# Kernel optimization log

Hardware: AMD Instinct MI355X
Metric: run time of the kernel (lower is better)

The kernel has to match this reference:

```python
import jax, jax.numpy as jnp
import numpy as np

CUTOFF = 5.0           # module init kwarg
NSYS, NAT = 64, 1000   # 64 systems of 1000 atoms each
BOX = 21.544           # cubic box edge -> ~0.1 atoms/A^3 (water-like density)
MAX_PAIRS = 2_200_000


def setup_inputs() -> dict:
    key = jax.random.key(0)
    coords = jax.random.uniform(key, (NSYS * NAT, 3), dtype=jnp.float32) * BOX
    isys = jnp.repeat(jnp.arange(NSYS, dtype=jnp.int32), NAT)
    natoms = jnp.full((NSYS,), NAT, dtype=jnp.int32)
    return {"coordinates": coords, "isys": isys, "natoms": natoms}


def reference(coordinates, isys, natoms):
    # Fixed-capacity cutoff neighbor list (no PBC branch), faithful to
    # GraphGeneratorFixed: half-list (i<j, same system), squared distances d12,
    # compacted into a MAX_PAIRS buffer padded with padding_value=N, then
    # symmetrized by concatenation.
    nsys = natoms.shape[0]
    n = coordinates.shape[0]
    nat = n // nsys                      # equal-sized systems (static)
    padding_value = n
    cutoff2 = jnp.float32(CUTOFF * CUTOFF)

    x = coordinates.reshape(nsys, nat, 3)                 # [S, nat, 3]
    sq = jnp.sum(x * x, axis=-1)                          # [S, nat]
    gram = jnp.einsum('sid,sjd->sij', x, x)               # [S, nat, nat]
    d12 = sq[:, :, None] + sq[:, None, :] - 2.0 * gram    # squared distances

    triu = jnp.triu(jnp.ones((nat, nat), dtype=bool), k=1)  # i < j half-list
    mask = (d12 < cutoff2) & triu[None, :, :]             # [S, nat, nat]
    mflat = mask.reshape(-1)                              # [S*nat*nat]
    npairs = jnp.sum(mflat)

    # stream-compaction: position of each kept pair in the output buffer
    pos = jnp.cumsum(mflat.astype(jnp.int32)) - 1
    sel = jnp.where(mflat, pos, MAX_PAIRS)                # OOB -> dropped
    flat_idx = jnp.arange(nsys * nat * nat, dtype=jnp.int32)
    idx_buf = jnp.full((MAX_PAIRS,), -1, dtype=jnp.int32).at[sel].set(
        flat_idx, mode='drop')

    valid = idx_buf >= 0
    ib = jnp.maximum(idx_buf, 0)
    s = ib // (nat * nat)
    rem = ib % (nat * nat)
    i = rem // nat
    j = rem % nat
    src = jnp.where(valid, s * nat + i, padding_value)
    dst = jnp.where(valid, s * nat + j, padding_value)
    d12_sel = jnp.where(valid, d12.reshape(-1)[ib], cutoff2)

    # symmetrize (directed graph), as in the original
    edge_src = jnp.concatenate([src, dst])
    edge_dst = jnp.concatenate([dst, src])
    d12_out = jnp.concatenate([d12_sel, d12_sel])
    return edge_src, edge_dst, d12_out, npairs
```

## Files before the change

kernel.cpp:

```cpp
#include <hip/hip_runtime.h>

#define NSYS 64
#define NAT  1000
#define NTOT (NSYS * NAT)
#define MP   2200000
#define CUT2 25.0f
#define PADV 64000.0f
#define SCAN_BLOCKS 250
#define CAP  104
#define EB   512
#define LCN  1152
#define NROWS 512
#define POSB  4096

__device__ __forceinline__ float dist2f(float xi, float yi, float zi,
                                        float xj, float yj, float zj) {
    float dx = xi - xj, dy = yi - yj, dz = zi - zj;
    return fmaf(dz, dz, fmaf(dy, dy, dx * dx));
}

__device__ __forceinline__ int mbcnt(unsigned long long m) {
    unsigned lo = __builtin_amdgcn_mbcnt_lo((unsigned)m, 0u);
    return (int)__builtin_amdgcn_mbcnt_hi((unsigned)(m >> 32), lo);
}

__device__ __forceinline__ int emit_group(uint2* __restrict__ q, int running,
                                          bool k, int j, int r, float d,
                                          unsigned long long m) {
    if (k) {
        int rank = running + mbcnt(m);
        if (rank < CAP)
            q[rank] = make_uint2((unsigned)(j - r), __float_as_uint(d));
    }
    return running + (int)__popcll(m);
}

__global__ __launch_bounds__(1024) void k_eval(const float* __restrict__ coords,
                                               int* __restrict__ counts,
                                               uint2* __restrict__ qbuf) {
    __shared__ float4 lc[LCN];
    int s      = blockIdx.x >> 3;
    int stripe = blockIdx.x & 7;
    const float* cs = coords + s * (NAT * 3);
    for (int a = threadIdx.x; a < LCN; a += 1024)
        lc[a] = (a < NAT)
              ? make_float4(cs[3 * a], cs[3 * a + 1], cs[3 * a + 2], 0.0f)
              : make_float4(1.0e30f, 1.0e30f, 1.0e30f, 0.0f);
    __syncthreads();
    int w    = threadIdx.x >> 6;
    int lane = threadIdx.x & 63;
    int W    = stripe * 16 + w;
#pragma unroll
    for (int t = 0; t < 2; t++) {
        int Q = t ? (255 - W) : W;
        if (Q > 249) continue;
        int r0 = Q * 4;
        float4 a0 = lc[r0];
        float4 a1 = lc[r0 + 1];
        float4 a2 = lc[r0 + 2];
        float4 a3 = lc[r0 + 3];
        int gb = __builtin_amdgcn_readfirstlane(s * NAT + r0);
        uint2* q0 = qbuf + (size_t)gb * CAP;
        uint2* q1 = q0 + CAP;
        uint2* q2 = q1 + CAP;
        uint2* q3 = q2 + CAP;
        int run0 = 0, run1 = 0, run2 = 0, run3 = 0;
        {
            int j = r0 + 1 + lane;
            float4 c = lc[j];
            float d0 = dist2f(a0.x, a0.y, a0.z, c.x, c.y, c.z);
            float d1 = dist2f(a1.x, a1.y, a1.z, c.x, c.y, c.z);
            float d2 = dist2f(a2.x, a2.y, a2.z, c.x, c.y, c.z);
            float d3 = dist2f(a3.x, a3.y, a3.z, c.x, c.y, c.z);
            bool in = j < NAT;
            bool k0 = in && (d0 < CUT2);
            bool k1 = in && (j > r0 + 1) && (d1 < CUT2);
            bool k2 = in && (j > r0 + 2) && (d2 < CUT2);
            bool k3 = in && (j > r0 + 3) && (d3 < CUT2);
            unsigned long long m0 = __ballot(k0);
            unsigned long long m1 = __ballot(k1);
            unsigned long long m2 = __ballot(k2);
            unsigned long long m3 = __ballot(k3);
            run0 = emit_group(q0, run0, k0, j, r0,     d0, m0);
            run1 = emit_group(q1, run1, k1, j, r0 + 1, d1, m1);
            run2 = emit_group(q2, run2, k2, j, r0 + 2, d2, m2);
            run3 = emit_group(q3, run3, k3, j, r0 + 3, d3, m3);
        }
        int jb = r0 + 65;
        for (; jb + 127 < NAT; jb += 128) {
            int j = jb + lane;
            float4 c0 = lc[j];
            float4 c1 = lc[j + 64];
            float d00 = dist2f(a0.x, a0.y, a0.z, c0.x, c0.y, c0.z);
            float d10 = dist2f(a1.x, a1.y, a1.z, c0.x, c0.y, c0.z);
            float d20 = dist2f(a2.x, a2.y, a2.z, c0.x, c0.y, c0.z);
            float d30 = dist2f(a3.x, a3.y, a3.z, c0.x, c0.y, c0.z);
            bool k00 = d00 < CUT2;
            bool k10 = d10 < CUT2;
            bool k20 = d20 < CUT2;
            bool k30 = d30 < CUT2;
            unsigned long long m00 = __ballot(k00);
            unsigned long long m10 = __ballot(k10);
            unsigned long long m20 = __ballot(k20);
            unsigned long long m30 = __ballot(k30);
            run0 = emit_group(q0, run0, k00, j, r0,     d00, m00);
            run1 = emit_group(q1, run1, k10, j, r0 + 1, d10, m10);
            run2 = emit_group(q2, run2, k20, j, r0 + 2, d20, m20);
            run3 = emit_group(q3, run3, k30, j, r0 + 3, d30, m30);
            float d01 = dist2f(a0.x, a0.y, a0.z, c1.x, c1.y, c1.z);
            float d11 = dist2f(a1.x, a1.y, a1.z, c1.x, c1.y, c1.z);
            float d21 = dist2f(a2.x, a2.y, a2.z, c1.x, c1.y, c1.z);
            float d31 = dist2f(a3.x, a3.y, a3.z, c1.x, c1.y, c1.z);
            bool k01 = d01 < CUT2;
            bool k11 = d11 < CUT2;
            bool k21 = d21 < CUT2;
            bool k31 = d31 < CUT2;
            unsigned long long m01 = __ballot(k01);
            unsigned long long m11 = __ballot(k11);
            unsigned long long m21 = __ballot(k21);
            unsigned long long m31 = __ballot(k31);
            run0 = emit_group(q0, run0, k01, j + 64, r0,     d01, m01);
            run1 = emit_group(q1, run1, k11, j + 64, r0 + 1, d11, m11);
            run2 = emit_group(q2, run2, k21, j + 64, r0 + 2, d21, m21);
            run3 = emit_group(q3, run3, k31, j + 64, r0 + 3, d31, m31);
        }
        for (; jb < NAT; jb += 64) {
            int j = jb + lane;
            float4 c = lc[j];
            float d0 = dist2f(a0.x, a0.y, a0.z, c.x, c.y, c.z);
            float d1 = dist2f(a1.x, a1.y, a1.z, c.x, c.y, c.z);
            float d2 = dist2f(a2.x, a2.y, a2.z, c.x, c.y, c.z);
            float d3 = dist2f(a3.x, a3.y, a3.z, c.x, c.y, c.z);
            bool in = j < NAT;
            bool k0 = in && (d0 < CUT2);
            bool k1 = in && (d1 < CUT2);
            bool k2 = in && (d2 < CUT2);
            bool k3 = in && (d3 < CUT2);
            unsigned long long m0 = __ballot(k0);
            unsigned long long m1 = __ballot(k1);
            unsigned long long m2 = __ballot(k2);
            unsigned long long m3 = __ballot(k3);
            run0 = emit_group(q0, run0, k0, j, r0,     d0, m0);
            run1 = emit_group(q1, run1, k1, j, r0 + 1, d1, m1);
            run2 = emit_group(q2, run2, k2, j, r0 + 2, d2, m2);
            run3 = emit_group(q3, run3, k3, j, r0 + 3, d3, m3);
        }
        if (lane == 0)
            *(int4*)(counts + gb) = make_int4(run0, run1, run2, run3);
    }
}

__global__ __launch_bounds__(256) void k_scan_a(const int* __restrict__ counts,
                                                int* __restrict__ offs,
                                                int* __restrict__ bsum) {
    __shared__ int wsum[4];
    int t = threadIdx.x, lane = t & 63, wid = t >> 6;
    int g = blockIdx.x * 256 + t;
    int v = counts[g];
    int x = v;
#pragma unroll
    for (int off = 1; off < 64; off <<= 1) {
        int u = __shfl_up(x, off);
        if (lane >= off) x += u;
    }
    if (lane == 63) wsum[wid] = x;
    __syncthreads();
    int base = 0;
    if (wid > 0) base += wsum[0];
    if (wid > 1) base += wsum[1];
    if (wid > 2) base += wsum[2];
    offs[g] = base + x - v;
    if (t == 255) bsum[blockIdx.x] = base + x;
}

__global__ __launch_bounds__(1024) void k_emit(const int* __restrict__ offs,
                                               const int* __restrict__ bsum,
                                               const uint2* __restrict__ qbuf,
                                               float* __restrict__ out) {
    __shared__ int bpre[256];
    __shared__ int lgoff[NROWS + 1];
    __shared__ int sh_r0, sh_tot;
    int t = threadIdx.x;
    int v = 0;
    if (t < 256) {
        v = (t < SCAN_BLOCKS) ? bsum[t] : 0;
        bpre[t] = v;
    }
    __syncthreads();
    for (int off = 1; off < 256; off <<= 1) {
        int u = 0;
        if (t < 256 && t >= off) u = bpre[t - off];
        __syncthreads();
        if (t < 256) bpre[t] += u;
        __syncthreads();
    }
    int incl = (t < 256) ? bpre[t] : 0;
    __syncthreads();
    if (t < 256) bpre[t] = incl - v;
    if (t == 255) sh_tot = incl;
    __syncthreads();
    int total = sh_tot;

    int p0 = blockIdx.x * POSB;
    if (t == 0) {
        int lo = 0, hi = NTOT;
        while (lo < hi) {
            int mid = (lo + hi + 1) >> 1;
            int g = (mid < NTOT) ? offs[mid] + bpre[mid >> 8] : total;
            if (g <= p0) lo = mid; else hi = mid - 1;
        }
        sh_r0 = lo;
    }
    __syncthreads();
    int r0 = sh_r0;
    if (t <= NROWS) {
        int r = r0 + t;
        lgoff[t] = (r < NTOT) ? offs[r] + bpre[r >> 8] : total;
    }
    __syncthreads();

    if (blockIdx.x == 0 && t == 0) out[6 * MP] = (float)total;
    int valid = total < MP ? total : MP;

    int p4 = p0 + t * 4;
    if (p4 >= MP) return;
    int k = 0;
    for (int step = 256; step; step >>= 1) {
        int nk = k + step;
        if (nk <= NROWS - 1 && lgoff[nk] <= p4) k = nk;
    }
    float fs[4], fd[4], dd[4];
#pragma unroll
    for (int e = 0; e < 4; e++) {
        int p = p4 + e;
        if (p < valid) {
            while (k < NROWS - 1 && lgoff[k + 1] <= p) k++;
            int row = r0 + k;
            int local = p - lgoff[k];
            if (local > CAP - 1) local = CAP - 1;
            uint2 rec = qbuf[(size_t)row * CAP + local];
            fs[e] = (float)row;
            fd[e] = (float)(row + (int)rec.x);
            dd[e] = __uint_as_float(rec.y);
        } else {
            fs[e] = PADV; fd[e] = PADV; dd[e] = CUT2;
        }
    }
    if (p4 + 4 <= MP) {
        float4 vs = {fs[0], fs[1], fs[2], fs[3]};
        float4 vd = {fd[0], fd[1], fd[2], fd[3]};
        float4 vv = {dd[0], dd[1], dd[2], dd[3]};
        *(float4*)(out + p4)          = vs;
        *(float4*)(out + MP + p4)     = vd;
        *(float4*)(out + 2 * MP + p4) = vd;
        *(float4*)(out + 3 * MP + p4) = vs;
        *(float4*)(out + 4 * MP + p4) = vv;
        *(float4*)(out + 5 * MP + p4) = vv;
    } else {
#pragma unroll
        for (int e = 0; e < 4; e++) {
            int p = p4 + e;
            if (p < MP) {
                out[p]          = fs[e];
                out[MP + p]     = fd[e];
                out[2 * MP + p] = fd[e];
                out[3 * MP + p] = fs[e];
                out[4 * MP + p] = dd[e];
                out[5 * MP + p] = dd[e];
            }
        }
    }
}

extern "C" void kernel_launch(void* const* d_in, const int* in_sizes, int n_in,
                              void* d_out, int out_size, void* d_ws, size_t ws_size,
                              hipStream_t stream) {
    const float* coords = (const float*)d_in[0];
    float* out = (float*)d_out;

    int*   counts = (int*)d_ws;
    int*   offs   = counts + NTOT;
    int*   bsum   = offs + NTOT;
    uint2* qbuf   = (uint2*)(bsum + 256);

    int emit_blocks = (MP + POSB - 1) / POSB;
    k_eval<<<EB, 1024, 0, stream>>>(coords, counts, qbuf);
    k_scan_a<<<SCAN_BLOCKS, 256, 0, stream>>>(counts, offs, bsum);
    k_emit<<<emit_blocks, 1024, 0, stream>>>(offs, bsum, qbuf, out);
}
```

Measured before the change: 108.3 us.

## Store 16-bit neighbor offsets and recompute distances in emit kernel

The intermediate per-row queue now holds a 16-bit column offset instead of an 8-byte (offset, distance) record, which cuts queue write and read traffic by a factor of four. The emit kernel recomputes the squared distance from the coordinates, which adds gathered coordinate loads that should mostly hit cache. The shared coordinate tile is padded further so the tail loop and its bounds checks can be dropped, and out-of-range columns are filtered by the sentinel coordinates instead. Recomputing the distance with a different formula than the reference may cause small rounding differences.

Result: no change. 106.3 us (-1.9%).

```diff
diff --git a/kernel.cpp b/kernel.cpp
--- a/kernel.cpp
+++ b/kernel.cpp
@@ -9,7 +9,7 @@
 #define SCAN_BLOCKS 250
 #define CAP  104
 #define EB   512
-#define LCN  1152
+#define LCN  1216
 #define NROWS 512
 #define POSB  4096
 
@@ -24,20 +24,20 @@
     return (int)__builtin_amdgcn_mbcnt_hi((unsigned)(m >> 32), lo);
 }
 
-__device__ __forceinline__ int emit_group(uint2* __restrict__ q, int running,
-                                          bool k, int j, int r, float d,
+__device__ __forceinline__ int emit_group(unsigned short* __restrict__ q,
+                                          int running, bool k, int dj,
                                           unsigned long long m) {
     if (k) {
         int rank = running + mbcnt(m);
         if (rank < CAP)
-            q[rank] = make_uint2((unsigned)(j - r), __float_as_uint(d));
+            q[rank] = (unsigned short)dj;
     }
     return running + (int)__popcll(m);
 }
 
 __global__ __launch_bounds__(1024) void k_eval(const float* __restrict__ coords,
                                                int* __restrict__ counts,
-                                               uint2* __restrict__ qbuf) {
+                                               unsigned short* __restrict__ qbuf) {
     __shared__ float4 lc[LCN];
     int s      = blockIdx.x >> 3;
     int stripe = blockIdx.x & 7;
@@ -60,10 +60,10 @@
         float4 a2 = lc[r0 + 2];
         float4 a3 = lc[r0 + 3];
         int gb = __builtin_amdgcn_readfirstlane(s * NAT + r0);
-        uint2* q0 = qbuf + (size_t)gb * CAP;
-        uint2* q1 = q0 + CAP;
-        uint2* q2 = q1 + CAP;
-        uint2* q3 = q2 + CAP;
+        unsigned short* q0 = qbuf + (size_t)gb * CAP;
+        unsigned short* q1 = q0 + CAP;
+        unsigned short* q2 = q1 + CAP;
+        unsigned short* q3 = q2 + CAP;
         int run0 = 0, run1 = 0, run2 = 0, run3 = 0;
         {
             int j = r0 + 1 + lane;
@@ -72,22 +72,20 @@
             float d1 = dist2f(a1.x, a1.y, a1.z, c.x, c.y, c.z);
             float d2 = dist2f(a2.x, a2.y, a2.z, c.x, c.y, c.z);
             float d3 = dist2f(a3.x, a3.y, a3.z, c.x, c.y, c.z);
-            bool in = j < NAT;
-            bool k0 = in && (d0 < CUT2);
-            bool k1 = in && (j > r0 + 1) && (d1 < CUT2);
-            bool k2 = in && (j > r0 + 2) && (d2 < CUT2);
-            bool k3 = in && (j > r0 + 3) && (d3 < CUT2);
+            bool k0 = d0 < CUT2;
+            bool k1 = (lane > 0) && (d1 < CUT2);
+            bool k2 = (lane > 1) && (d2 < CUT2);
+            bool k3 = (lane > 2) && (d3 < CUT2);
             unsigned long long m0 = __ballot(k0);
             unsigned long long m1 = __ballot(k1);
             unsigned long long m2 = __ballot(k2);
             unsigned long long m3 = __ballot(k3);
-            run0 = emit_group(q0, run0, k0, j, r0,     d0, m0);
-            run1 = emit_group(q1, run1, k1, j, r0 + 1, d1, m1);
-            run2 = emit_group(q2, run2, k2, j, r0 + 2, d2, m2);
-            run3 = emit_group(q3, run3, k3, j, r0 + 3, d3, m3);
-        }
-        int jb = r0 + 65;
-        for (; jb + 127 < NAT; jb += 128) {
+            run0 = emit_group(q0, run0, k0, j - r0,     m0);
+            run1 = emit_group(q1, run1, k1, j - r0 - 1, m1);
+            run2 = emit_group(q2, run2, k2, j - r0 - 2, m2);
+            run3 = emit_group(q3, run3, k3, j - r0 - 3, m3);
+        }
+        for (int jb = r0 + 65; jb < NAT; jb += 128) {
             int j = jb + lane;
             float4 c0 = lc[j];
             float4 c1 = lc[j + 64];
@@ -103,10 +101,10 @@
             unsigned long long m10 = __ballot(k10);
             unsigned long long m20 = __ballot(k20);
             unsigned long long m30 = __ballot(k30);
-            run0 = emit_group(q0, run0, k00, j, r0,     d00, m00);
-            run1 = emit_group(q1, run1, k10, j, r0 + 1, d10, m10);
-            run2 = emit_group(q2, run2, k20, j, r0 + 2, d20, m20);
-            run3 = emit_group(q3, run3, k30, j, r0 + 3, d30, m30);
+            run0 = emit_group(q0, run0, k00, j - r0,     m00);
+            run1 = emit_group(q1, run1, k10, j - r0 - 1, m10);
+            run2 = emit_group(q2, run2, k20, j - r0 - 2, m20);
+            run3 = emit_group(q3, run3, k30, j - r0 - 3, m30);
             float d01 = dist2f(a0.x, a0.y, a0.z, c1.x, c1.y, c1.z);
             float d11 = dist2f(a1.x, a1.y, a1.z, c1.x, c1.y, c1.z);
             float d21 = dist2f(a2.x, a2.y, a2.z, c1.x, c1.y, c1.z);
@@ -119,31 +117,10 @@
             unsigned long long m11 = __ballot(k11);
             unsigned long long m21 = __ballot(k21);
             unsigned long long m31 = __ballot(k31);
-            run0 = emit_group(q0, run0, k01, j + 64, r0,     d01, m01);
-            run1 = emit_group(q1, run1, k11, j + 64, r0 + 1, d11, m11);
-            run2 = emit_group(q2, run2, k21, j + 64, r0 + 2, d21, m21);
-            run3 = emit_group(q3, run3, k31, j + 64, r0 + 3, d31, m31);
-        }
-        for (; jb < NAT; jb += 64) {
-            int j = jb + lane;
-            float4 c = lc[j];
-            float d0 = dist2f(a0.x, a0.y, a0.z, c.x, c.y, c.z);
-            float d1 = dist2f(a1.x, a1.y, a1.z, c.x, c.y, c.z);
-            float d2 = dist2f(a2.x, a2.y, a2.z, c.x, c.y, c.z);
-            float d3 = dist2f(a3.x, a3.y, a3.z, c.x, c.y, c.z);
-            bool in = j < NAT;
-            bool k0 = in && (d0 < CUT2);
-            bool k1 = in && (d1 < CUT2);
-            bool k2 = in && (d2 < CUT2);
-            bool k3 = in && (d3 < CUT2);
-            unsigned long long m0 = __ballot(k0);
-            unsigned long long m1 = __ballot(k1);
-            unsigned long long m2 = __ballot(k2);
-            unsigned long long m3 = __ballot(k3);
-            run0 = emit_group(q0, run0, k0, j, r0,     d0, m0);
-            run1 = emit_group(q1, run1, k1, j, r0 + 1, d1, m1);
-            run2 = emit_group(q2, run2, k2, j, r0 + 2, d2, m2);
-            run3 = emit_group(q3, run3, k3, j, r0 + 3, d3, m3);
+            run0 = emit_group(q0, run0, k01, j + 64 - r0,     m01);
+            run1 = emit_group(q1, run1, k11, j + 64 - r0 - 1, m11);
+            run2 = emit_group(q2, run2, k21, j + 64 - r0 - 2, m21);
+            run3 = emit_group(q3, run3, k31, j + 64 - r0 - 3, m31);
         }
         if (lane == 0)
             *(int4*)(counts + gb) = make_int4(run0, run1, run2, run3);
@@ -173,9 +150,10 @@
     if (t == 255) bsum[blockIdx.x] = base + x;
 }
 
-__global__ __launch_bounds__(1024) void k_emit(const int* __restrict__ offs,
+__global__ __launch_bounds__(1024) void k_emit(const float* __restrict__ coords,
+                                               const int* __restrict__ offs,
                                                const int* __restrict__ bsum,
-                                               const uint2* __restrict__ qbuf,
+                                               const unsigned short* __restrict__ qbuf,
                                                float* __restrict__ out) {
     __shared__ int bpre[256];
     __shared__ int lgoff[NROWS + 1];
@@ -238,10 +216,13 @@
             int row = r0 + k;
             int local = p - lgoff[k];
             if (local > CAP - 1) local = CAP - 1;
-            uint2 rec = qbuf[(size_t)row * CAP + local];
+            int dj = qbuf[(size_t)row * CAP + local];
+            int col = row + dj;
+            const float* cr = coords + 3 * row;
+            const float* cj = coords + 3 * col;
             fs[e] = (float)row;
-            fd[e] = (float)(row + (int)rec.x);
-            dd[e] = __uint_as_float(rec.y);
+            fd[e] = (float)col;
+            dd[e] = dist2f(cr[0], cr[1], cr[2], cj[0], cj[1], cj[2]);
         } else {
             fs[e] = PADV; fd[e] = PADV; dd[e] = CUT2;
         }
@@ -278,13 +259,13 @@
     const float* coords = (const float*)d_in[0];
     float* out = (float*)d_out;
 
-    int*   counts = (int*)d_ws;
-    int*   offs   = counts + NTOT;
-    int*   bsum   = offs + NTOT;
-    uint2* qbuf   = (uint2*)(bsum + 256);
+    int*            counts = (int*)d_ws;
+    int*            offs   = counts + NTOT;
+    int*            bsum   = offs + NTOT;
+    unsigned short* qbuf   = (unsigned short*)(bsum + 256);
 
     int emit_blocks = (MP + POSB - 1) / POSB;
     k_eval<<<EB, 1024, 0, stream>>>(coords, counts, qbuf);
     k_scan_a<<<SCAN_BLOCKS, 256, 0, stream>>>(counts, offs, bsum);
-    k_emit<<<emit_blocks, 1024, 0, stream>>>(offs, bsum, qbuf, out);
-}
+    k_emit<<<emit_blocks, 1024, 0, stream>>>(coords, offs, bsum, qbuf, out);
+}
```
